# Kernel optimization log

Hardware: AMD Instinct MI355X
Metric: run time of the kernel (lower is better)

Reference implementation:

```python
import jax, jax.numpy as jnp
import numpy as np

EPS_NORM = 1e-12
BN_EPS = 1e-5
TEMP = 0.07


def _l2norm(x, axis):
    n = jnp.sqrt(jnp.sum(x * x, axis=axis, keepdims=True))
    return x / jnp.maximum(n, EPS_NORM)


def _bn_eval(z, w, b):
    # inference-mode BatchNorm2d with running_mean=0, running_var=1
    s = w / jnp.sqrt(jnp.asarray(1.0 + BN_EPS, z.dtype))
    return z * s[None, :, None, None] + b[None, :, None, None]


def setup_inputs() -> dict:
    key = jax.random.key(0)
    ks = jax.random.split(key, 8)
    B, C, H, W = 16, 256, 64, 64
    KD, P = 128, 256
    x = jax.random.normal(ks[0], (B, C, H, W), jnp.float32)
    m_features = jax.random.normal(ks[1], (P, KD), jnp.float32)
    q_w = jax.random.normal(ks[2], (KD, C), jnp.float32) * 0.05
    k_w = jax.random.normal(ks[3], (KD, KD), jnp.float32) * 0.05
    v_w = jax.random.normal(ks[4], (KD, KD), jnp.float32) * 0.05
    o_w = jax.random.normal(ks[5], (C, KD), jnp.float32) * 0.05
    dw_w = jax.random.normal(ks[6], (C, 1, 3, 3), jnp.float32) * 0.1
    return {
        "x": x, "m_features": m_features,
        "q_w": q_w, "q_b": jnp.zeros((KD,), jnp.float32),
        "k_w": k_w, "k_b": jnp.zeros((KD,), jnp.float32),
        "v_w": v_w, "v_b": jnp.zeros((KD,), jnp.float32),
        "o_w": o_w, "o_b": jnp.zeros((C,), jnp.float32),
        "dw_w": dw_w,
        "bn1_w": jnp.ones((C,), jnp.float32), "bn1_b": jnp.zeros((C,), jnp.float32),
        "bn2_w": jnp.ones((C,), jnp.float32), "bn2_b": jnp.zeros((C,), jnp.float32),
        "gamma": jnp.ones((C,), jnp.float32) * 1e-5,
    }


def reference(x, m_features, q_w, q_b, k_w, k_b, v_w, v_b, o_w, o_b,
              dw_w, bn1_w, bn1_b, bn2_w, bn2_b, gamma):
    B, C, H, W = x.shape
    KD = q_w.shape[0]
    residual = x
    # q_proj 1x1 conv -> [B,KD,H,W], L2-normalize over channel dim
    q = jnp.einsum('bchw,kc->bkhw', x, q_w) + q_b[None, :, None, None]
    q = _l2norm(q, axis=1)
    q = q.reshape(B, KD, H * W).transpose(0, 2, 1)  # [B, HW, KD]
    # k/v projections of memory bank [P, KD]
    k = _l2norm(m_features @ k_w.T + k_b, axis=-1)
    v = m_features @ v_w.T + v_b
    # fp32 attention with clamped logits
    q32, k32, v32 = q.astype(jnp.float32), k.astype(jnp.float32), v.astype(jnp.float32)
    logits = jnp.clip(jnp.einsum('bnd,pd->bnp', q32, k32) / TEMP, -30.0, 30.0)
    attn = jax.nn.softmax(logits, axis=-1)
    out = jnp.einsum('bnp,pd->bnd', attn, v32).astype(x.dtype)
    out = out.transpose(0, 2, 1).reshape(B, KD, H, W)
    # out_proj 1x1 conv -> [B,C,H,W]
    out = jnp.einsum('bkhw,ck->bchw', out, o_w) + o_b[None, :, None, None]
    # local branch: depthwise 3x3 conv + BN + exact GELU
    local = jax.lax.conv_general_dilated(
        out, dw_w, window_strides=(1, 1), padding='SAME',
        feature_group_count=C,
        dimension_numbers=('NCHW', 'OIHW', 'NCHW'))
    local = jax.nn.gelu(_bn_eval(local, bn1_w, bn1_b), approximate=False)
    out = out + local
    return _bn_eval(residual + out * gamma[None, :, None, None], bn2_w, bn2_b)
```

## Files before the change

kernel.cpp:

```cpp
#include <hip/hip_runtime.h>
#include <hip/hip_bf16.h>
#include <math.h>

#define B_ 16
#define C_ 256
#define H_ 64
#define W_ 64
#define KD_ 128
#define P_ 256
#define HW_ (H_ * W_)

typedef __bf16 bf16;
typedef float f32x4_t __attribute__((ext_vector_type(4)));
typedef float f32x16_t __attribute__((ext_vector_type(16)));
typedef unsigned char u8;

__device__ __forceinline__ unsigned cvt_pk_fp8_lo(float a, float b, unsigned old) {
#if __has_builtin(__builtin_amdgcn_cvt_pk_fp8_f32)
    return __builtin_amdgcn_cvt_pk_fp8_f32(a, b, old, false);
#else
    unsigned r = old;
    asm("v_cvt_pk_fp8_f32 %0, %1, %2" : "+v"(r) : "v"(a), "v"(b));
    return r;
#endif
}
__device__ __forceinline__ unsigned cvt_pk_fp8_hi(float a, float b, unsigned old) {
#if __has_builtin(__builtin_amdgcn_cvt_pk_fp8_f32)
    return __builtin_amdgcn_cvt_pk_fp8_f32(a, b, old, true);
#else
    unsigned r = old;
    asm("v_cvt_pk_fp8_f32 %0, %1, %2 op_sel:[0,0,1]" : "+v"(r) : "v"(a), "v"(b));
    return r;
#endif
}
__device__ __forceinline__ uint2 pack8_fp8(const float* f) {
    uint2 r;
    r.x = cvt_pk_fp8_hi(f[2], f[3], cvt_pk_fp8_lo(f[0], f[1], 0u));
    r.y = cvt_pk_fp8_hi(f[6], f[7], cvt_pk_fp8_lo(f[4], f[5], 0u));
    return r;
}
template<int SEL>
__device__ __forceinline__ float fp8_to_f32(unsigned w) {
#if __has_builtin(__builtin_amdgcn_cvt_f32_fp8)
    return __builtin_amdgcn_cvt_f32_fp8(w, SEL);
#else
    float r;
    asm("v_cvt_f32_fp8 %0, %1" : "=v"(r) : "v"(w >> (SEL * 8)));
    return r;
#endif
}
template<typename T>
__device__ __forceinline__ void nt_store(T* p, T v) {
#if __has_builtin(__builtin_nontemporal_store)
    __builtin_nontemporal_store(v, p);
#else
    *p = v;
#endif
}

__global__ __launch_bounds__(512, 8) void k_pre_a(
    const float* __restrict__ x, u8* __restrict__ x8,
    const float* __restrict__ m_feat,
    const float* __restrict__ k_w, const float* __restrict__ k_b,
    const float* __restrict__ v_w, const float* __restrict__ v_b,
    float* __restrict__ kn_f, float* __restrict__ v_f)
{
    __shared__ __align__(16) u8 tile[16 * 2048];
    __shared__ float msh4[4][KD_];
    __shared__ float red4[4][2];
    const int u = blockIdx.x;
    const int t = threadIdx.x;

    if (u < 512) {
        const int b    = u >> 5;
        const int v_   = u & 31;
        const int cblk = v_ >> 1;
        const int ph   = v_ & 1;
        {
            const int cl = t >> 5, sub = t & 31;
            const float* src = x + ((size_t)b * C_ + cblk * 16 + cl) * HW_ + ph * 2048;
#pragma unroll
            for (int i = 0; i < 16; ++i) {
                const f32x4_t v = *(const f32x4_t*)(src + (i * 32 + sub) * 4);
                const unsigned w = cvt_pk_fp8_hi(v[2], v[3],
                                   cvt_pk_fp8_lo(v[0], v[1], 0u));
                *(unsigned*)&tile[cl * 2048 + (i * 32 + sub) * 4] = w;
            }
        }
        __syncthreads();
        {
            const int pr = t & 63;
            const int r0 = t >> 6;
#pragma unroll
            for (int it = 0; it < 4; ++it) {
                const int r = it * 8 + r0;
                const int lp = r * 64 + pr;
                union { u8 bytes[16]; uint4 uu; } g;
#pragma unroll
                for (int c = 0; c < 16; ++c) g.bytes[c] = tile[c * 2048 + lp];
                const int h = ph * 32 + r;
                *(uint4*)(x8 + (((size_t)(b * 64 + h) * 16 + cblk) << 10) + pr * 16) = g.uu;
            }
        }
    } else {
        const int sub = t >> 7;
        const int j   = t & 127;
        const int p   = (u - 512) * 4 + sub;
        msh4[sub][j] = m_feat[p * KD_ + j];
        __syncthreads();

        float ka = k_b[j];
        float va = v_b[j];
#pragma unroll 4
        for (int d = 0; d < KD_; ++d) {
            const float m = msh4[sub][d];
            ka = fmaf(m, k_w[j * KD_ + d], ka);
            va = fmaf(m, v_w[j * KD_ + d], va);
        }
        float s = ka * ka;
#pragma unroll
        for (int o = 1; o < 64; o <<= 1) s += __shfl_xor(s, o);
        if ((j & 63) == 0) red4[sub][j >> 6] = s;
        __syncthreads();
        s = red4[sub][0] + red4[sub][1];
        const float inv = 1.0f / (0.07f * fmaxf(sqrtf(s), 1e-12f));
        kn_f[p * KD_ + j] = ka * inv;
        v_f[p * KD_ + j] = va;
    }
}

__global__ __launch_bounds__(256) void k_prep23(
    const float* __restrict__ o_w, const float* __restrict__ v_f,
    const float* __restrict__ q_w, const float* __restrict__ kn_f,
    u8* __restrict__ m28, u8* __restrict__ qw8, u8* __restrict__ kn8)
{
    if (blockIdx.x < 256) {
        const int c = blockIdx.x;
        const int p = threadIdx.x;
        __shared__ float osh[KD_];
        if (p < KD_) osh[p] = o_w[c * KD_ + p];
        __syncthreads();
        float acc = 0.f;
#pragma unroll 4
        for (int k = 0; k < KD_; ++k) acc = fmaf(osh[k], v_f[p * KD_ + k], acc);
        const int mt = c >> 5, r = c & 31;
        const int ks = p >> 4, sub = (p >> 3) & 1, jj = p & 7;
        const unsigned pk = cvt_pk_fp8_lo(acc * 16.0f, 0.f, 0u);
        m28[(((mt * 16 + ks) * 64) + sub * 32 + r) * 8 + jj] = (u8)(pk & 0xffu);
    } else {
        const int t = (blockIdx.x - 256) * 256 + threadIdx.x;
        float f[8];
        if (t < 4096) {
            const int lane = t & 63, g = t >> 6, mt = g >> 4, ks = g & 15;
            const int row = mt * 32 + (lane & 31), k0 = ks * 16 + (lane >> 5) * 8;
            const float* src = q_w + row * C_ + k0;
#pragma unroll
            for (int j = 0; j < 8; ++j) f[j] = src[j] * 16.0f;
            ((uint2*)qw8)[t] = pack8_fp8(f);
        } else {
            const int u = t - 4096;
            const int lane = u & 63, g = u >> 6, mt = g >> 3, ks = g & 7;
            const int row = mt * 32 + (lane & 31), k0 = ks * 16 + (lane >> 5) * 8;
            const float* src = kn_f + row * KD_ + k0;
#pragma unroll
            for (int j = 0; j < 8; ++j) f[j] = src[j];
            ((uint2*)kn8)[u] = pack8_fp8(f);
        }
    }
}

__global__ __launch_bounds__(512, 4) void k_attn(
    const u8* __restrict__ x8,
    const float* __restrict__ q_b, const float* __restrict__ o_b,
    const u8* __restrict__ qw8, const u8* __restrict__ kn8,
    const u8* __restrict__ m28, u8* __restrict__ outf8)
{
    __shared__ __align__(16) char lds[43008];
    char* const ebuf = lds;
    char* const qbuf = lds + 16384;
    float* const ss_lds   = (float*)(lds + 32768);
    float* const pmax_lds = (float*)(lds + 34816);
    float* const sum_lds  = (float*)(lds + 38912);

    const int rp = blockIdx.x;
    const int b = blockIdx.y;
    const int tid = threadIdx.x;
    const int lane = tid & 63;
    const int wid = tid >> 6;
    const int l31 = lane & 31;
    const int kh  = lane >> 5;

    long kna[8];
#pragma unroll
    for (int ks = 0; ks < 8; ++ks)
        kna[ks] = *(const long*)(kn8 + ((wid * 8 + ks) * 64 + lane) * 8);

    const int mtA = wid & 3, nh = wid >> 2;
    {
        const u8* xrow = x8 + ((size_t)(b * 64 + rp * 2 + nh) << 14);
        f32x16_t qacc0, qacc1;
#pragma unroll
        for (int i = 0; i < 16; ++i) { qacc0[i] = 0.f; qacc1[i] = 0.f; }
#pragma unroll
        for (int ks = 0; ks < 16; ++ks) {
            const long a = *(const long*)(qw8 + ((mtA * 16 + ks) * 64 + lane) * 8);
            const long bx0 = *(const long*)(xrow + ks * 1024 + l31 * 16 + kh * 8);
            const long bx1 = *(const long*)(xrow + ks * 1024 + (32 + l31) * 16 + kh * 8);
            qacc0 = __builtin_amdgcn_mfma_f32_32x32x16_fp8_fp8(a, bx0, qacc0, 0, 0, 0);
            qacc1 = __builtin_amdgcn_mfma_f32_32x32x16_fp8_fp8(a, bx1, qacc1, 0, 0, 0);
        }
#pragma unroll
        for (int nt = 0; nt < 2; ++nt) {
            const int pix = nh * 64 + nt * 32 + l31;
            float ssp = 0.f;
#pragma unroll
            for (int g = 0; g < 4; ++g) {
                const f32x4_t qbv = *(const f32x4_t*)(q_b + mtA * 32 + g * 8 + kh * 4);
#pragma unroll
                for (int i = 0; i < 4; ++i) {
                    float qv = (nt == 0) ? qacc0[g * 4 + i] : qacc1[g * 4 + i];
                    qv += 16.0f * qbv[i];
                    if (nt == 0) qacc0[g * 4 + i] = qv; else qacc1[g * 4 + i] = qv;
                    ssp = fmaf(qv, qv, ssp);
                }
            }
            ssp += __shfl_xor(ssp, 32);
            if (lane < 32) ss_lds[pix * 4 + mtA] = ssp;
#pragma unroll
            for (int g = 0; g < 4; ++g) {
                const float e0 = (nt == 0) ? qacc0[g * 4 + 0] : qacc1[g * 4 + 0];
                const float e1 = (nt == 0) ? qacc0[g * 4 + 1] : qacc1[g * 4 + 1];
                const float e2 = (nt == 0) ? qacc0[g * 4 + 2] : qacc1[g * 4 + 2];
                const float e3 = (nt == 0) ? qacc0[g * 4 + 3] : qacc1[g * 4 + 3];
                const unsigned qw_ = cvt_pk_fp8_hi(e2, e3, cvt_pk_fp8_lo(e0, e1, 0u));
                *(unsigned*)(qbuf + pix * 128 +
                             ((mtA * 32 + g * 8 + kh * 4) ^ ((l31 & 15) << 3))) = qw_;
            }
        }
    }
    __syncthreads();

    f32x16_t lacc0, lacc1, lacc2, lacc3;
#pragma unroll
    for (int i = 0; i < 16; ++i) { lacc0[i] = 0.f; lacc1[i] = 0.f; lacc2[i] = 0.f; lacc3[i] = 0.f; }
#pragma unroll
    for (int ks = 0; ks < 8; ++ks) {
        const int ko = (ks * 16 + kh * 8) ^ ((l31 & 15) << 3);
        const long bq0 = *(const long*)(qbuf + (0 * 32 + l31) * 128 + ko);
        const long bq1 = *(const long*)(qbuf + (1 * 32 + l31) * 128 + ko);
        const long bq2 = *(const long*)(qbuf + (2 * 32 + l31) * 128 + ko);
        const long bq3 = *(const long*)(qbuf + (3 * 32 + l31) * 128 + ko);
        lacc0 = __builtin_amdgcn_mfma_f32_32x32x16_fp8_fp8(kna[ks], bq0, lacc0, 0, 0, 0);
        lacc1 = __builtin_amdgcn_mfma_f32_32x32x16_fp8_fp8(kna[ks], bq1, lacc1, 0, 0, 0);
        lacc2 = __builtin_amdgcn_mfma_f32_32x32x16_fp8_fp8(kna[ks], bq2, lacc2, 0, 0, 0);
        lacc3 = __builtin_amdgcn_mfma_f32_32x32x16_fp8_fp8(kna[ks], bq3, lacc3, 0, 0, 0);
    }
#pragma unroll
    for (int nt = 0; nt < 4; ++nt) {
        const int pix = nt * 32 + l31;
        float mx = -1e30f;
#pragma unroll
        for (int i = 0; i < 16; ++i) {
            const float lv = (nt == 0) ? lacc0[i] : (nt == 1) ? lacc1[i]
                           : (nt == 2) ? lacc2[i] : lacc3[i];
            mx = fmaxf(mx, lv);
        }
        mx = fmaxf(mx, __shfl_xor(mx, 32));
        if (lane < 32) pmax_lds[pix * 8 + wid] = mx;
    }
    __syncthreads();

#pragma unroll
    for (int nt = 0; nt < 4; ++nt) {
        const int pix = nt * 32 + l31;
        const f32x4_t s4 = *(const f32x4_t*)(ss_lds + pix * 4);
        const float qinv = 1.0f / fmaxf(sqrtf(s4[0] + s4[1] + s4[2] + s4[3]), 1e-12f);
        const f32x4_t ma = *(const f32x4_t*)(pmax_lds + pix * 8);
        const f32x4_t mb = *(const f32x4_t*)(pmax_lds + pix * 8 + 4);
        const float cof = 5.545177444479562f -
                          fmaxf(fmaxf(fmaxf(ma[0], ma[1]), fmaxf(ma[2], ma[3])),
                                fmaxf(fmaxf(mb[0], mb[1]), fmaxf(mb[2], mb[3]))) * qinv;
        float sm = 0.f;
#pragma unroll
        for (int g = 0; g < 4; ++g) {
            float e[4];
#pragma unroll
            for (int i = 0; i < 4; ++i) {
                const float lv = (nt == 0) ? lacc0[g * 4 + i] : (nt == 1) ? lacc1[g * 4 + i]
                               : (nt == 2) ? lacc2[g * 4 + i] : lacc3[g * 4 + i];
                e[i] = __expf(fmaf(lv, qinv, cof));
                sm += e[i];
            }
            const unsigned ew = cvt_pk_fp8_hi(e[2], e[3],
                                cvt_pk_fp8_lo(e[0], e[1], 0u));
            const int p0 = wid * 32 + g * 8 + kh * 4;
            *(unsigned*)(ebuf + pix * 256 + (p0 ^ (l31 << 3))) = ew;
        }
        sm += __shfl_xor(sm, 32);
        if (lane < 32) sum_lds[pix * 8 + wid] = sm;
    }
    __syncthreads();

    f32x16_t oacc0, oacc1, oacc2, oacc3;
#pragma unroll
    for (int i = 0; i < 16; ++i) { oacc0[i] = 0.f; oacc1[i] = 0.f; oacc2[i] = 0.f; oacc3[i] = 0.f; }
#pragma unroll
    for (int ks = 0; ks < 16; ++ks) {
        const long a = *(const long*)(m28 + ((wid * 16 + ks) * 64 + lane) * 8);
        const int ko = (ks * 16 + kh * 8);
        const long be0 = *(const long*)(ebuf + (0 * 32 + l31) * 256 + (ko ^ (l31 << 3)));
        const long be1 = *(const long*)(ebuf + (1 * 32 + l31) * 256 + (ko ^ (l31 << 3)));
        const long be2 = *(const long*)(ebuf + (2 * 32 + l31) * 256 + (ko ^ (l31 << 3)));
        const long be3 = *(const long*)(ebuf + (3 * 32 + l31) * 256 + (ko ^ (l31 << 3)));
        oacc0 = __builtin_amdgcn_mfma_f32_32x32x16_fp8_fp8(a, be0, oacc0, 0, 0, 0);
        oacc1 = __builtin_amdgcn_mfma_f32_32x32x16_fp8_fp8(a, be1, oacc1, 0, 0, 0);
        oacc2 = __builtin_amdgcn_mfma_f32_32x32x16_fp8_fp8(a, be2, oacc2, 0, 0, 0);
        oacc3 = __builtin_amdgcn_mfma_f32_32x32x16_fp8_fp8(a, be3, oacc3, 0, 0, 0);
    }
    {
        u8* const obase = outf8 + (size_t)b * C_ * HW_ + rp * 128;
        f32x4_t obv16[4];
#pragma unroll
        for (int g = 0; g < 4; ++g) {
            const f32x4_t t = *(const f32x4_t*)(o_b + wid * 32 + g * 8 + kh * 4);
            obv16[g] = t * 16.0f;
        }
#pragma unroll
        for (int nt = 0; nt < 4; ++nt) {
            const int p = nt * 32 + l31;
            const f32x4_t sa = *(const f32x4_t*)(sum_lds + p * 8);
            const f32x4_t sb = *(const f32x4_t*)(sum_lds + p * 8 + 4);
            const float rs16 = 1.0f / ((sa[0] + sa[1] + sa[2] + sa[3]) +
                                       (sb[0] + sb[1] + sb[2] + sb[3]));
            u8* const op = obase + p;
#pragma unroll
            for (int g = 0; g < 4; ++g) {
                float o[4];
#pragma unroll
                for (int i = 0; i < 4; ++i) {
                    const float av = (nt == 0) ? oacc0[g * 4 + i] : (nt == 1) ? oacc1[g * 4 + i]
                                   : (nt == 2) ? oacc2[g * 4 + i] : oacc3[g * 4 + i];
                    o[i] = fmaf(av, rs16, obv16[g][i]);
                }
                const unsigned u01 = cvt_pk_fp8_lo(o[0], o[1], 0u);
                const unsigned u23 = cvt_pk_fp8_lo(o[2], o[3], 0u);
                const int c = wid * 32 + g * 8 + kh * 4;
                op[(size_t)(c + 0) * HW_] = (u8)(u01 & 0xff);
                op[(size_t)(c + 1) * HW_] = (u8)((u01 >> 8) & 0xff);
                op[(size_t)(c + 2) * HW_] = (u8)(u23 & 0xff);
                op[(size_t)(c + 3) * HW_] = (u8)((u23 >> 8) & 0xff);
            }
        }
    }
}

__global__ __launch_bounds__(256, 8) void k_post(
    const float* __restrict__ x, const u8* __restrict__ outf8,
    const float* __restrict__ dw_w,
    const float* __restrict__ bn1_w, const float* __restrict__ bn1_b,
    const float* __restrict__ bn2_w, const float* __restrict__ bn2_b,
    const float* __restrict__ gamma, float* __restrict__ y)
{
    __shared__ __align__(16) u8 os8[64 + HW_ + 64];
    u8* const os = os8 + 64;
    const int bc = blockIdx.x;
    const int c = bc & (C_ - 1);
    const int tid = threadIdx.x;

    if (tid < 4)       *(uint4*)&os8[tid * 16] = make_uint4(0, 0, 0, 0);
    else if (tid < 8)  *(uint4*)&os8[64 + HW_ + (tid - 4) * 16] = make_uint4(0, 0, 0, 0);
    *(uint4*)&os[tid * 16] = *(const uint4*)(outf8 + (size_t)bc * HW_ + tid * 16);

    const float cbn = 0.99999500003750f;
    const float s1 = bn1_w[c] * cbn, b1 = bn1_b[c];
    const float s2 = bn2_w[c] * cbn, b2 = bn2_b[c];
    const float g = gamma[c];
    const float gc = g * 0.0625f;
    float kw[9];
#pragma unroll
    for (int j = 0; j < 9; ++j) kw[j] = dw_w[c * 9 + j] * 0.0625f;

    __syncthreads();

    const int q = tid & 15;
    const int c4 = q * 4;
    const int r0 = tid >> 4;
    const float* xc = x + (size_t)bc * HW_;
    float* yc = y + (size_t)bc * HW_;

#pragma unroll
    for (int k = 0; k < 4; ++k) {
        const int r = r0 + k * 16;
        const f32x4_t x4 = *(const f32x4_t*)(xc + r * 64 + c4);
        float vt[6], vm[6], vb[6];
        {
            const int rbt = r * 64, rbm = rbt + 64, rbb = rbt + 128;
            const unsigned uCt = *(const unsigned*)&os8[rbt + c4];
            const unsigned uCm = *(const unsigned*)&os8[rbm + c4];
            const unsigned uCb = *(const unsigned*)&os8[rbb + c4];
            vt[1] = fp8_to_f32<0>(uCt); vt[2] = fp8_to_f32<1>(uCt);
            vt[3] = fp8_to_f32<2>(uCt); vt[4] = fp8_to_f32<3>(uCt);
            vm[1] = fp8_to_f32<0>(uCm); vm[2] = fp8_to_f32<1>(uCm);
            vm[3] = fp8_to_f32<2>(uCm); vm[4] = fp8_to_f32<3>(uCm);
            vb[1] = fp8_to_f32<0>(uCb); vb[2] = fp8_to_f32<1>(uCb);
            vb[3] = fp8_to_f32<2>(uCb); vb[4] = fp8_to_f32<3>(uCb);
            if (q > 0) {
                vt[0] = fp8_to_f32<3>(*(const unsigned*)&os8[rbt + c4 - 4]);
                vm[0] = fp8_to_f32<3>(*(const unsigned*)&os8[rbm + c4 - 4]);
                vb[0] = fp8_to_f32<3>(*(const unsigned*)&os8[rbb + c4 - 4]);
            } else { vt[0] = vm[0] = vb[0] = 0.f; }
            if (q < 15) {
                vt[5] = fp8_to_f32<0>(*(const unsigned*)&os8[rbt + c4 + 4]);
                vm[5] = fp8_to_f32<0>(*(const unsigned*)&os8[rbm + c4 + 4]);
                vb[5] = fp8_to_f32<0>(*(const unsigned*)&os8[rbb + c4 + 4]);
            } else { vt[5] = vm[5] = vb[5] = 0.f; }
        }
        f32x4_t y4;
#pragma unroll
        for (int j = 0; j < 4; ++j) {
            float conv = kw[0] * vt[j];
            conv = fmaf(kw[1], vt[j + 1], conv);
            conv = fmaf(kw[2], vt[j + 2], conv);
            conv = fmaf(kw[3], vm[j], conv);
            conv = fmaf(kw[4], vm[j + 1], conv);
            conv = fmaf(kw[5], vm[j + 2], conv);
            conv = fmaf(kw[6], vb[j], conv);
            conv = fmaf(kw[7], vb[j + 1], conv);
            conv = fmaf(kw[8], vb[j + 2], conv);
            const float t = fmaf(conv, s1, b1);
            const float lg = t / (1.0f + __expf(-1.702f * t));
            y4[j] = fmaf(lg, g, fmaf(vm[j + 1], gc, x4[j])) * s2 + b2;
        }
        nt_store((f32x4_t*)(yc + r * 64 + c4), y4);
    }
}

extern "C" void kernel_launch(void* const* d_in, const int* in_sizes, int n_in,
                              void* d_out, int out_size, void* d_ws, size_t ws_size,
                              hipStream_t stream)
{
    const float* x     = (const float*)d_in[0];
    const float* m_f   = (const float*)d_in[1];
    const float* q_w   = (const float*)d_in[2];
    const float* q_b   = (const float*)d_in[3];
    const float* k_w   = (const float*)d_in[4];
    const float* k_b   = (const float*)d_in[5];
    const float* v_w   = (const float*)d_in[6];
    const float* v_b   = (const float*)d_in[7];
    const float* o_w   = (const float*)d_in[8];
    const float* o_b   = (const float*)d_in[9];
    const float* dw_w  = (const float*)d_in[10];
    const float* bn1_w = (const float*)d_in[11];
    const float* bn1_b = (const float*)d_in[12];
    const float* bn2_w = (const float*)d_in[13];
    const float* bn2_b = (const float*)d_in[14];
    const float* gamma = (const float*)d_in[15];

    char* ws = (char*)d_ws;
    u8*    qw8   = (u8*)(ws);
    u8*    kn8   = (u8*)(ws + (32 << 10));
    u8*    m28   = (u8*)(ws + (64 << 10));
    u8*    x8    = (u8*)(ws + (1 << 20));
    u8*    outf8 = (u8*)(ws + (17 << 20));
    float* kn_f  = (float*)(ws + (34 << 20));
    float* v_f   = (float*)(ws + (34 << 20) + (128 << 10));

    k_pre_a<<<dim3(576), dim3(512), 0, stream>>>(x, x8, m_f, k_w, k_b, v_w, v_b,
                                                 kn_f, v_f);
    k_prep23<<<dim3(288), dim3(256), 0, stream>>>(o_w, v_f, q_w, kn_f,
                                                  m28, qw8, kn8);
    k_attn<<<dim3(H_ / 2, B_), dim3(512), 0, stream>>>(x8, q_b, o_b, qw8, kn8,
                                                       m28, outf8);
    k_post<<<dim3(B_ * C_), dim3(256), 0, stream>>>(
        x, outf8, dw_w, bn1_w, bn1_b, bn2_w, bn2_b, gamma, (float*)d_out);
}
```

Measured before the change: 86.52 us.

## Replace per-pixel softmax max reduction with constant bound from unit-norm logits

Drops the row-max pass in the attention kernel, including its cross-wave LDS exchange and a block barrier. It uses a fixed exponent offset instead, which is safe because q and k are L2-normalised, so each logit is bounded by 1/TEMP. The k-operand fragments are now loaded inside the MFMA loop instead of being held in registers, the LDS layout is enlarged, k_post launch bounds are lowered, and the output store becomes a normal store instead of a nontemporal one. The larger LDS footprint may reduce how many attention blocks fit on a CU at once.

```diff
diff --git a/kernel.cpp b/kernel.cpp
--- a/kernel.cpp
+++ b/kernel.cpp
@@ -47,14 +47,6 @@
     float r;
     asm("v_cvt_f32_fp8 %0, %1" : "=v"(r) : "v"(w >> (SEL * 8)));
     return r;
-#endif
-}
-template<typename T>
-__device__ __forceinline__ void nt_store(T* p, T v) {
-#if __has_builtin(__builtin_nontemporal_store)
-    __builtin_nontemporal_store(v, p);
-#else
-    *p = v;
 #endif
 }
 
@@ -175,12 +167,11 @@
     const u8* __restrict__ qw8, const u8* __restrict__ kn8,
     const u8* __restrict__ m28, u8* __restrict__ outf8)
 {
-    __shared__ __align__(16) char lds[43008];
+    __shared__ __align__(16) char lds[55296];
     char* const ebuf = lds;
-    char* const qbuf = lds + 16384;
-    float* const ss_lds   = (float*)(lds + 32768);
-    float* const pmax_lds = (float*)(lds + 34816);
-    float* const sum_lds  = (float*)(lds + 38912);
+    char* const qbuf = lds + 32768;
+    float* const ss_lds  = (float*)(lds + 49152);
+    float* const sum_lds = (float*)(lds + 51200);
 
     const int rp = blockIdx.x;
     const int b = blockIdx.y;
@@ -189,11 +180,6 @@
     const int wid = tid >> 6;
     const int l31 = lane & 31;
     const int kh  = lane >> 5;
-
-    long kna[8];
-#pragma unroll
-    for (int ks = 0; ks < 8; ++ks)
-        kna[ks] = *(const long*)(kn8 + ((wid * 8 + ks) * 64 + lane) * 8);
 
     const int mtA = wid & 3, nh = wid >> 2;
     {
@@ -245,41 +231,24 @@
     for (int i = 0; i < 16; ++i) { lacc0[i] = 0.f; lacc1[i] = 0.f; lacc2[i] = 0.f; lacc3[i] = 0.f; }
 #pragma unroll
     for (int ks = 0; ks < 8; ++ks) {
+        const long a = *(const long*)(kn8 + ((wid * 8 + ks) * 64 + lane) * 8);
         const int ko = (ks * 16 + kh * 8) ^ ((l31 & 15) << 3);
         const long bq0 = *(const long*)(qbuf + (0 * 32 + l31) * 128 + ko);
         const long bq1 = *(const long*)(qbuf + (1 * 32 + l31) * 128 + ko);
         const long bq2 = *(const long*)(qbuf + (2 * 32 + l31) * 128 + ko);
         const long bq3 = *(const long*)(qbuf + (3 * 32 + l31) * 128 + ko);
-        lacc0 = __builtin_amdgcn_mfma_f32_32x32x16_fp8_fp8(kna[ks], bq0, lacc0, 0, 0, 0);
-        lacc1 = __builtin_amdgcn_mfma_f32_32x32x16_fp8_fp8(kna[ks], bq1, lacc1, 0, 0, 0);
-        lacc2 = __builtin_amdgcn_mfma_f32_32x32x16_fp8_fp8(kna[ks], bq2, lacc2, 0, 0, 0);
-        lacc3 = __builtin_amdgcn_mfma_f32_32x32x16_fp8_fp8(kna[ks], bq3, lacc3, 0, 0, 0);
-    }
-#pragma unroll
-    for (int nt = 0; nt < 4; ++nt) {
-        const int pix = nt * 32 + l31;
-        float mx = -1e30f;
-#pragma unroll
-        for (int i = 0; i < 16; ++i) {
-            const float lv = (nt == 0) ? lacc0[i] : (nt == 1) ? lacc1[i]
-                           : (nt == 2) ? lacc2[i] : lacc3[i];
-            mx = fmaxf(mx, lv);
-        }
-        mx = fmaxf(mx, __shfl_xor(mx, 32));
-        if (lane < 32) pmax_lds[pix * 8 + wid] = mx;
-    }
-    __syncthreads();
+        lacc0 = __builtin_amdgcn_mfma_f32_32x32x16_fp8_fp8(a, bq0, lacc0, 0, 0, 0);
+        lacc1 = __builtin_amdgcn_mfma_f32_32x32x16_fp8_fp8(a, bq1, lacc1, 0, 0, 0);
+        lacc2 = __builtin_amdgcn_mfma_f32_32x32x16_fp8_fp8(a, bq2, lacc2, 0, 0, 0);
+        lacc3 = __builtin_amdgcn_mfma_f32_32x32x16_fp8_fp8(a, bq3, lacc3, 0, 0, 0);
+    }
 
 #pragma unroll
     for (int nt = 0; nt < 4; ++nt) {
         const int pix = nt * 32 + l31;
         const f32x4_t s4 = *(const f32x4_t*)(ss_lds + pix * 4);
         const float qinv = 1.0f / fmaxf(sqrtf(s4[0] + s4[1] + s4[2] + s4[3]), 1e-12f);
-        const f32x4_t ma = *(const f32x4_t*)(pmax_lds + pix * 8);
-        const f32x4_t mb = *(const f32x4_t*)(pmax_lds + pix * 8 + 4);
-        const float cof = 5.545177444479562f -
-                          fmaxf(fmaxf(fmaxf(ma[0], ma[1]), fmaxf(ma[2], ma[3])),
-                                fmaxf(fmaxf(mb[0], mb[1]), fmaxf(mb[2], mb[3]))) * qinv;
+        const float cof = -8.740536912452074f;
         float sm = 0.f;
 #pragma unroll
         for (int g = 0; g < 4; ++g) {
@@ -307,7 +276,7 @@
 #pragma unroll
     for (int ks = 0; ks < 16; ++ks) {
         const long a = *(const long*)(m28 + ((wid * 16 + ks) * 64 + lane) * 8);
-        const int ko = (ks * 16 + kh * 8);
+        const int ko = ks * 16 + kh * 8;
         const long be0 = *(const long*)(ebuf + (0 * 32 + l31) * 256 + (ko ^ (l31 << 3)));
         const long be1 = *(const long*)(ebuf + (1 * 32 + l31) * 256 + (ko ^ (l31 << 3)));
         const long be2 = *(const long*)(ebuf + (2 * 32 + l31) * 256 + (ko ^ (l31 << 3)));
@@ -330,8 +299,8 @@
             const int p = nt * 32 + l31;
             const f32x4_t sa = *(const f32x4_t*)(sum_lds + p * 8);
             const f32x4_t sb = *(const f32x4_t*)(sum_lds + p * 8 + 4);
-            const float rs16 = 1.0f / ((sa[0] + sa[1] + sa[2] + sa[3]) +
-                                       (sb[0] + sb[1] + sb[2] + sb[3]));
+            const float rs = 1.0f / ((sa[0] + sa[1] + sa[2] + sa[3]) +
+                                     (sb[0] + sb[1] + sb[2] + sb[3]));
             u8* const op = obase + p;
 #pragma unroll
             for (int g = 0; g < 4; ++g) {
@@ -340,7 +309,7 @@
                 for (int i = 0; i < 4; ++i) {
                     const float av = (nt == 0) ? oacc0[g * 4 + i] : (nt == 1) ? oacc1[g * 4 + i]
                                    : (nt == 2) ? oacc2[g * 4 + i] : oacc3[g * 4 + i];
-                    o[i] = fmaf(av, rs16, obv16[g][i]);
+                    o[i] = fmaf(av, rs, obv16[g][i]);
                 }
                 const unsigned u01 = cvt_pk_fp8_lo(o[0], o[1], 0u);
                 const unsigned u23 = cvt_pk_fp8_lo(o[2], o[3], 0u);
@@ -354,7 +323,7 @@
     }
 }
 
-__global__ __launch_bounds__(256, 8) void k_post(
+__global__ __launch_bounds__(256, 4) void k_post(
     const float* __restrict__ x, const u8* __restrict__ outf8,
     const float* __restrict__ dw_w,
     const float* __restrict__ bn1_w, const float* __restrict__ bn1_b,
@@ -431,7 +400,7 @@
             const float lg = t / (1.0f + __expf(-1.702f * t));
             y4[j] = fmaf(lg, g, fmaf(vm[j + 1], gc, x4[j])) * s2 + b2;
         }
-        nt_store((f32x4_t*)(yc + r * 64 + c4), y4);
+        *(f32x4_t*)(yc + r * 64 + c4) = y4;
     }
 }
 
```

Measured after the change: 88.96 us. 2.8% more time.
